# Optimization experiments

Measured on AMD Instinct MI355X. Metric: run time of the kernel, lower is better.

## Reference

```python
import jax, jax.numpy as jnp
import numpy as np

CHANNELS = 128


def setup_inputs() -> dict:
    key = jax.random.key(0)
    ks = jax.random.split(key, 7)
    B, N, C, E = 1, 50000, CHANNELS, 800000
    in_dim = 2 * C + 2  # channels*2 + 2
    tokens = jax.random.normal(ks[0], (B, N, C), dtype=jnp.float32)
    coords = jax.random.normal(ks[1], (B, N, 2), dtype=jnp.float32)
    edge_index = jax.random.randint(ks[2], (2, E), 0, N, dtype=jnp.int64)
    # MLP params: Linear(in_dim, C) -> ReLU -> Linear(C, 1)
    w1 = jax.random.normal(ks[3], (in_dim, C), dtype=jnp.float32) / np.sqrt(in_dim)
    b1 = jnp.zeros((C,), dtype=jnp.float32)
    w2 = jax.random.normal(ks[4], (C, 1), dtype=jnp.float32) / np.sqrt(C)
    b2 = jnp.zeros((1,), dtype=jnp.float32)
    return {"tokens": tokens, "coords": coords, "edge_index": edge_index,
            "w1": w1, "b1": b1, "w2": w2, "b2": b2}


def reference(tokens, coords, edge_index, w1, b1, w2, b2):
    src = edge_index[0]
    dst = edge_index[1]
    x_src = tokens[:, src, :]               # [B, E, C]
    x_dst = tokens[:, dst, :]               # [B, E, C]
    delta = coords[:, dst, :] - coords[:, src, :]  # [B, E, 2]
    feat = jnp.concatenate([x_src, x_dst, delta], axis=-1)  # [B, E, 2C+2]
    h = jax.nn.relu(jnp.einsum('bef,fh->beh', feat, w1) + b1)  # [B, E, C]
    return jnp.einsum('beh,ho->beo', h, w2) + b2               # [B, E, 1]
```

## Files before the change

kernel.cpp:

```cpp
#include <hip/hip_runtime.h>

static constexpr int CH   = 128;
static constexpr int KPAD = 192;

typedef __attribute__((ext_vector_type(8))) short bf16x8;
typedef __attribute__((ext_vector_type(4))) float f32x4;
typedef __attribute__((ext_vector_type(4))) unsigned int u32x4;

__device__ inline unsigned short f2bf(float x) {
    unsigned int u = __float_as_uint(x);
    unsigned int r = (u + 0x7fffu + ((u >> 16) & 1u)) >> 16;
    return (unsigned short)r;
}
__device__ inline unsigned int pack2bf(float a, float b) {
    return (unsigned int)f2bf(a) | ((unsigned int)f2bf(b) << 16);
}

__global__ __launch_bounds__(256) void idx_prep(
    const unsigned int* __restrict__ idxw, uint2* __restrict__ idx2,
    long long E, long long Epad) {
    unsigned nz = 0;
    const int lane = threadIdx.x & 63;
    for (int i = lane; i < 128; i += 64) nz |= idxw[2 * i + 1];
    const int is64 = (__ballot(nz != 0u) == 0ULL) ? 1 : 0;
    const long long stride = (long long)gridDim.x * blockDim.x;
    for (long long i = (long long)blockIdx.x * blockDim.x + threadIdx.x;
         i < Epad; i += stride) {
        uint2 v = make_uint2(0u, 0u);
        if (i < E) {
            const unsigned s = is64 ? idxw[2 * i] : idxw[i];
            const unsigned d = is64 ? idxw[2 * (E + i)] : idxw[E + i];
            v = make_uint2(s << 8, d << 8);
        }
        idx2[i] = v;
    }
}

__global__ __launch_bounds__(256) void w1_prep2(const float* __restrict__ w1,
                                                const float* __restrict__ b1,
                                                unsigned short* __restrict__ Wf) {
    const int gid = blockIdx.x * 256 + threadIdx.x;
    if (gid >= 4 * 5 * 4 * 64) return;
    const int lane = gid & 63;
    const int seg  = gid >> 6;
    const int m    = seg & 3;
    const int ks   = (seg >> 2) % 5;
    const int w    = seg / 20;
    const int c    = w * 64 + m * 16 + (lane & 15);
    const int k0   = ks * 32 + (lane >> 4) * 8;
    const bool isQ = c >= 128;
    const int cc   = c & 127;
    const float sgn = isQ ? 1.f : -1.f;
    unsigned int out[4];
#pragma unroll
    for (int h = 0; h < 4; ++h) {
        float v[2];
#pragma unroll
        for (int j = 0; j < 2; ++j) {
            const int k = k0 + 2 * h + j;
            float x;
            if (k < 128)       x = isQ ? w1[(size_t)(128 + k) * CH + cc]
                                       : w1[(size_t)k * CH + cc];
            else if (k == 128) x = sgn * w1[(size_t)(2 * CH) * CH + cc];
            else if (k == 129) x = sgn * w1[(size_t)(2 * CH + 1) * CH + cc];
            else if (k == 130) x = isQ ? b1[cc] : 0.f;
            else               x = 0.f;
            v[j] = x;
        }
        out[h] = pack2bf(v[0], v[1]);
    }
    *(uint4*)&Wf[(size_t)gid * 8] = make_uint4(out[0], out[1], out[2], out[3]);
}

__global__ __launch_bounds__(256) void node_mfma4(
    const float* __restrict__ tokens, const float* __restrict__ coords,
    const unsigned short* __restrict__ Wf, unsigned short* __restrict__ Pb,
    unsigned short* __restrict__ Qb, int N) {
    __shared__ unsigned short Atile[32 * KPAD];

    const int t    = threadIdx.x;
    const int l    = t & 63;
    const int wid  = t >> 6;
    const int n0   = blockIdx.x * 32;
    const int woff = wid * 64;
    const int bl   = l & 15;
    const int bh   = l >> 4;

#pragma unroll
    for (int it = 0; it < 2; ++it) {
        const int idx  = it * 256 + t;
        const int node = idx >> 4;
        const int cq   = idx & 15;
        float4 v0 = make_float4(0.f, 0.f, 0.f, 0.f);
        float4 v1 = v0;
        if (n0 + node < N) {
            const float* src = &tokens[(size_t)(n0 + node) * CH + cq * 8];
            v0 = *(const float4*)src;
            v1 = *(const float4*)(src + 4);
        }
        uint4 u;
        u.x = pack2bf(v0.x, v0.y);
        u.y = pack2bf(v0.z, v0.w);
        u.z = pack2bf(v1.x, v1.y);
        u.w = pack2bf(v1.z, v1.w);
        const int byte = node * 384 + ((cq * 16) ^ ((node & 7) << 4));
        *(uint4*)((char*)Atile + byte) = u;
    }
    {
        const int node = t >> 3;
        const int ce   = t & 7;
        uint4 u = make_uint4(0u, 0u, 0u, 0u);
        if (ce == 0 && n0 + node < N) {
            const float cx = coords[2 * (n0 + node)];
            const float cy = coords[2 * (n0 + node) + 1];
            u.x = pack2bf(cx, cy);
            u.y = pack2bf(1.f, 0.f);
        }
        const int byte = node * 384 + (((16 + ce) * 16) ^ ((node & 7) << 4));
        *(uint4*)((char*)Atile + byte) = u;
    }
    __syncthreads();

    f32x4 acc[4][2];
#pragma unroll
    for (int m = 0; m < 4; ++m)
#pragma unroll
        for (int n = 0; n < 2; ++n) acc[m][n] = (f32x4){0.f, 0.f, 0.f, 0.f};

#pragma unroll
    for (int ks = 0; ks < 5; ++ks) {
        bf16x8 wfrag[4], tfrag[2];
#pragma unroll
        for (int m = 0; m < 4; ++m)
            wfrag[m] = *(const bf16x8*)&Wf[(size_t)(((wid * 5 + ks) * 4 + m) * 64
                                                    + l) * 8];
#pragma unroll
        for (int n = 0; n < 2; ++n) {
            const int row  = n * 16 + bl;
            const int byte = row * 384 + ((ks * 64 + bh * 16) ^ ((row & 7) << 4));
            tfrag[n] = *(const bf16x8*)((const char*)Atile + byte);
        }
#pragma unroll
        for (int m = 0; m < 4; ++m)
#pragma unroll
            for (int n = 0; n < 2; ++n)
                acc[m][n] = __builtin_amdgcn_mfma_f32_16x16x32_bf16(
                    wfrag[m], tfrag[n], acc[m][n], 0, 0, 0);
    }

#pragma unroll
    for (int m = 0; m < 4; ++m) {
        const int c  = woff + m * 16 + bh * 4;
        const int cc = c & (CH - 1);
        unsigned short* dst = (c < CH) ? Pb : Qb;
#pragma unroll
        for (int n = 0; n < 2; ++n) {
            const int node = n0 + n * 16 + bl;
            if (node < N) {
                uint2 val;
                val.x = pack2bf(acc[m][n][0], acc[m][n][1]);
                val.y = pack2bf(acc[m][n][2], acc[m][n][3]);
                *(uint2*)&dst[(size_t)node * CH + cc] = val;
            }
        }
    }
}

__global__ __launch_bounds__(256) void edge_g16x8(
    const unsigned int* __restrict__ idx2, const char* __restrict__ Pb,
    const char* __restrict__ Qb, const float* __restrict__ w2,
    const float* __restrict__ b2, float* __restrict__ out, long long E) {
    const int t  = threadIdx.x;
    const int gl = t & 15;
    const long long nch = (E + 7) >> 3;
    const long long g0  = (long long)blockIdx.x * 16 + (t >> 4);
    const long long ng  = (long long)gridDim.x * 16;
    const float4 w2a = *(const float4*)&w2[8 * gl];
    const float4 w2b = *(const float4*)&w2[8 * gl + 4];
    const float bias = b2[0];

    for (long long chk = g0; chk < nch; chk += ng) {
        const long long e0 = chk << 3;
        const u32x4* ip = (const u32x4*)&idx2[e0 * 2];
        const u32x4 i0 = __builtin_nontemporal_load(ip);
        const u32x4 i1 = __builtin_nontemporal_load(ip + 1);
        const u32x4 i2 = __builtin_nontemporal_load(ip + 2);
        const u32x4 i3 = __builtin_nontemporal_load(ip + 3);
        const unsigned soff[8] = {i0.x, i0.z, i1.x, i1.z, i2.x, i2.z, i3.x, i3.z};
        const unsigned doff[8] = {i0.y, i0.w, i1.y, i1.w, i2.y, i2.w, i3.y, i3.w};
        uint4 pv[8], qv[8];
#pragma unroll
        for (int j = 0; j < 8; ++j)
            pv[j] = *(const uint4*)(Pb + soff[j] + 16 * gl);
#pragma unroll
        for (int j = 0; j < 8; ++j)
            qv[j] = *(const uint4*)(Qb + doff[j] + 16 * gl);

        float part[8];
#pragma unroll
        for (int j = 0; j < 8; ++j) {
            float acc = 0.f;
            const unsigned pw[4] = {pv[j].x, pv[j].y, pv[j].z, pv[j].w};
            const unsigned qw[4] = {qv[j].x, qv[j].y, qv[j].z, qv[j].w};
            const float wv[8] = {w2a.x, w2a.y, w2a.z, w2a.w,
                                 w2b.x, w2b.y, w2b.z, w2b.w};
#pragma unroll
            for (int wdx = 0; wdx < 4; ++wdx) {
                const float plo = __uint_as_float(pw[wdx] << 16);
                const float phi = __uint_as_float(pw[wdx] & 0xffff0000u);
                const float qlo = __uint_as_float(qw[wdx] << 16);
                const float qhi = __uint_as_float(qw[wdx] & 0xffff0000u);
                const float hlo = fmaxf(plo + qlo, 0.f);
                const float hhi = fmaxf(phi + qhi, 0.f);
                acc = fmaf(hlo, wv[2 * wdx], acc);
                acc = fmaf(hhi, wv[2 * wdx + 1], acc);
            }
            part[j] = acc;
        }

        float t0 = part[0] + __shfl_xor(part[0], 1);
        float t1 = part[1] + __shfl_xor(part[1], 1);
        float t2 = part[2] + __shfl_xor(part[2], 1);
        float t3 = part[3] + __shfl_xor(part[3], 1);
        float t4 = part[4] + __shfl_xor(part[4], 1);
        float t5 = part[5] + __shfl_xor(part[5], 1);
        float t6 = part[6] + __shfl_xor(part[6], 1);
        float t7 = part[7] + __shfl_xor(part[7], 1);
        float a0 = (gl & 1) ? t1 : t0;
        float a1 = (gl & 1) ? t3 : t2;
        float a2 = (gl & 1) ? t5 : t4;
        float a3 = (gl & 1) ? t7 : t6;
        a0 += __shfl_xor(a0, 2);
        a1 += __shfl_xor(a1, 2);
        a2 += __shfl_xor(a2, 2);
        a3 += __shfl_xor(a3, 2);
        float b0  = (gl & 2) ? a1 : a0;
        float b1v = (gl & 2) ? a3 : a2;
        b0  += __shfl_xor(b0, 4);
        b1v += __shfl_xor(b1v, 4);
        float c = (gl & 4) ? b1v : b0;
        c += __shfl_xor(c, 8);

        if (gl < 8 && e0 + gl < E) out[e0 + gl] = c + bias;
    }
}

extern "C" void kernel_launch(void* const* d_in, const int* in_sizes, int n_in,
                              void* d_out, int out_size, void* d_ws,
                              size_t ws_size, hipStream_t stream) {
    const float* tokens = (const float*)d_in[0];
    const float* coords = (const float*)d_in[1];
    const unsigned int* idxw = (const unsigned int*)d_in[2];
    const float* w1 = (const float*)d_in[3];
    const float* b1 = (const float*)d_in[4];
    const float* w2 = (const float*)d_in[5];
    const float* b2 = (const float*)d_in[6];
    float* out = (float*)d_out;

    const int N = in_sizes[0] / CH;
    const long long E = in_sizes[2] / 2;
    const long long Epad = ((E + 7) >> 3) << 3;

    unsigned short* Pb = (unsigned short*)d_ws;
    unsigned short* Qb = Pb + (size_t)N * CH;
    uint2* idx2 = (uint2*)(Qb + (size_t)N * CH);
    unsigned short* Wf = (unsigned short*)(idx2 + Epad);

    idx_prep<<<1024, 256, 0, stream>>>(idxw, idx2, E, Epad);
    w1_prep2<<<20, 256, 0, stream>>>(w1, b1, Wf);

    node_mfma4<<<(N + 31) / 32, 256, 0, stream>>>(tokens, coords, Wf, Pb, Qb, N);

    edge_g16x8<<<2048, 256, 0, stream>>>((const unsigned int*)idx2,
                                         (const char*)Pb, (const char*)Qb,
                                         w2, b2, out, E);
}
```

Baseline: 81.59 us.

## Split node features into channel halves and gather edges in two passes

Node projections P and Q are written as two 64-channel halves each, and the edge kernel runs twice, once per half, accumulating through a partial buffer. The aim is a smaller random-gather working set per pass for better cache hit rates. In exchange, the index array is read twice, an extra launch is added, and a partial-sum buffer is written and reread.

Measured after the change: 77.45 us. 1.05x faster.

```diff
diff --git a/kernel.cpp b/kernel.cpp
--- a/kernel.cpp
+++ b/kernel.cpp
@@ -5,7 +5,7 @@
 
 typedef __attribute__((ext_vector_type(8))) short bf16x8;
 typedef __attribute__((ext_vector_type(4))) float f32x4;
-typedef __attribute__((ext_vector_type(4))) unsigned int u32x4;
+typedef __attribute__((ext_vector_type(2))) unsigned int u32x2;
 
 __device__ inline unsigned short f2bf(float x) {
     unsigned int u = __float_as_uint(x);
@@ -30,7 +30,7 @@
         if (i < E) {
             const unsigned s = is64 ? idxw[2 * i] : idxw[i];
             const unsigned d = is64 ? idxw[2 * (E + i)] : idxw[E + i];
-            v = make_uint2(s << 8, d << 8);
+            v = make_uint2(s << 7, d << 7);
         }
         idx2[i] = v;
     }
@@ -72,17 +72,17 @@
     *(uint4*)&Wf[(size_t)gid * 8] = make_uint4(out[0], out[1], out[2], out[3]);
 }
 
-__global__ __launch_bounds__(256) void node_mfma4(
+__global__ __launch_bounds__(256) void node_mfma5(
     const float* __restrict__ tokens, const float* __restrict__ coords,
-    const unsigned short* __restrict__ Wf, unsigned short* __restrict__ Pb,
-    unsigned short* __restrict__ Qb, int N) {
+    const unsigned short* __restrict__ Wf, unsigned short* __restrict__ Plo,
+    unsigned short* __restrict__ Phi, unsigned short* __restrict__ Qlo,
+    unsigned short* __restrict__ Qhi, int N) {
     __shared__ unsigned short Atile[32 * KPAD];
 
     const int t    = threadIdx.x;
     const int l    = t & 63;
     const int wid  = t >> 6;
     const int n0   = blockIdx.x * 32;
-    const int woff = wid * 64;
     const int bl   = l & 15;
     const int bh   = l >> 4;
 
@@ -148,11 +148,11 @@
                     wfrag[m], tfrag[n], acc[m][n], 0, 0, 0);
     }
 
+    unsigned short* dst = (wid == 0) ? Plo : (wid == 1) ? Phi
+                          : (wid == 2) ? Qlo : Qhi;
 #pragma unroll
     for (int m = 0; m < 4; ++m) {
-        const int c  = woff + m * 16 + bh * 4;
-        const int cc = c & (CH - 1);
-        unsigned short* dst = (c < CH) ? Pb : Qb;
+        const int col = m * 16 + bh * 4;
 #pragma unroll
         for (int n = 0; n < 2; ++n) {
             const int node = n0 + n * 16 + bl;
@@ -160,60 +160,62 @@
                 uint2 val;
                 val.x = pack2bf(acc[m][n][0], acc[m][n][1]);
                 val.y = pack2bf(acc[m][n][2], acc[m][n][3]);
-                *(uint2*)&dst[(size_t)node * CH + cc] = val;
+                *(uint2*)&dst[(size_t)node * 64 + col] = val;
             }
         }
     }
 }
 
-__global__ __launch_bounds__(256) void edge_g16x8(
-    const unsigned int* __restrict__ idx2, const char* __restrict__ Pb,
-    const char* __restrict__ Qb, const float* __restrict__ w2,
-    const float* __restrict__ b2, float* __restrict__ out, long long E) {
+template <int PASS>
+__global__ __launch_bounds__(256) void edge_pass(
+    const unsigned int* __restrict__ idx2w, const unsigned short* __restrict__ Pb,
+    const unsigned short* __restrict__ Qb, const float* __restrict__ w2,
+    const float* __restrict__ b2, float* __restrict__ partial,
+    float* __restrict__ out, long long E) {
     const int t  = threadIdx.x;
-    const int gl = t & 15;
-    const long long nch = (E + 7) >> 3;
-    const long long g0  = (long long)blockIdx.x * 16 + (t >> 4);
-    const long long ng  = (long long)gridDim.x * 16;
-    const float4 w2a = *(const float4*)&w2[8 * gl];
-    const float4 w2b = *(const float4*)&w2[8 * gl + 4];
+    const int gl = t & 7;
+    const long long nq = (E + 3) >> 2;
+    const long long g0 = (long long)blockIdx.x * 32 + (t >> 3);
+    const long long ng = (long long)gridDim.x * 32;
+    const float4 wa = *(const float4*)&w2[PASS * 64 + gl * 8];
+    const float4 wb = *(const float4*)&w2[PASS * 64 + gl * 8 + 4];
     const float bias = b2[0];
-
-    for (long long chk = g0; chk < nch; chk += ng) {
-        const long long e0 = chk << 3;
-        const u32x4* ip = (const u32x4*)&idx2[e0 * 2];
-        const u32x4 i0 = __builtin_nontemporal_load(ip);
-        const u32x4 i1 = __builtin_nontemporal_load(ip + 1);
-        const u32x4 i2 = __builtin_nontemporal_load(ip + 2);
-        const u32x4 i3 = __builtin_nontemporal_load(ip + 3);
-        const unsigned soff[8] = {i0.x, i0.z, i1.x, i1.z, i2.x, i2.z, i3.x, i3.z};
-        const unsigned doff[8] = {i0.y, i0.w, i1.y, i1.w, i2.y, i2.w, i3.y, i3.w};
-        uint4 pv[8], qv[8];
-#pragma unroll
-        for (int j = 0; j < 8; ++j)
-            pv[j] = *(const uint4*)(Pb + soff[j] + 16 * gl);
-#pragma unroll
-        for (int j = 0; j < 8; ++j)
-            qv[j] = *(const uint4*)(Qb + doff[j] + 16 * gl);
-
-        float part[8];
-#pragma unroll
-        for (int j = 0; j < 8; ++j) {
-            float acc = 0.f;
+    const char* P = (const char*)Pb;
+    const char* Q = (const char*)Qb;
+
+    for (long long q = g0; q < nq; q += ng) {
+        const long long e0 = q << 2;
+        const u32x2 iv = __builtin_nontemporal_load(
+            (const u32x2*)&idx2w[(e0 + (gl & 3)) * 2]);
+        unsigned soff[4], doff[4];
+#pragma unroll
+        for (int j = 0; j < 4; ++j) {
+            soff[j] = __shfl(iv.x, j, 8);
+            doff[j] = __shfl(iv.y, j, 8);
+        }
+        uint4 pv[4], qv[4];
+#pragma unroll
+        for (int j = 0; j < 4; ++j)
+            pv[j] = *(const uint4*)(P + soff[j] + 16 * gl);
+#pragma unroll
+        for (int j = 0; j < 4; ++j)
+            qv[j] = *(const uint4*)(Q + doff[j] + 16 * gl);
+
+        float part[4];
+#pragma unroll
+        for (int j = 0; j < 4; ++j) {
+            const float wv[8] = {wa.x, wa.y, wa.z, wa.w, wb.x, wb.y, wb.z, wb.w};
             const unsigned pw[4] = {pv[j].x, pv[j].y, pv[j].z, pv[j].w};
             const unsigned qw[4] = {qv[j].x, qv[j].y, qv[j].z, qv[j].w};
-            const float wv[8] = {w2a.x, w2a.y, w2a.z, w2a.w,
-                                 w2b.x, w2b.y, w2b.z, w2b.w};
-#pragma unroll
-            for (int wdx = 0; wdx < 4; ++wdx) {
-                const float plo = __uint_as_float(pw[wdx] << 16);
-                const float phi = __uint_as_float(pw[wdx] & 0xffff0000u);
-                const float qlo = __uint_as_float(qw[wdx] << 16);
-                const float qhi = __uint_as_float(qw[wdx] & 0xffff0000u);
-                const float hlo = fmaxf(plo + qlo, 0.f);
-                const float hhi = fmaxf(phi + qhi, 0.f);
-                acc = fmaf(hlo, wv[2 * wdx], acc);
-                acc = fmaf(hhi, wv[2 * wdx + 1], acc);
+            float acc = 0.f;
+#pragma unroll
+            for (int i = 0; i < 4; ++i) {
+                const float plo = __uint_as_float(pw[i] << 16);
+                const float phi = __uint_as_float(pw[i] & 0xffff0000u);
+                const float qlo = __uint_as_float(qw[i] << 16);
+                const float qhi = __uint_as_float(qw[i] & 0xffff0000u);
+                acc = fmaf(fmaxf(plo + qlo, 0.f), wv[2 * i], acc);
+                acc = fmaf(fmaxf(phi + qhi, 0.f), wv[2 * i + 1], acc);
             }
             part[j] = acc;
         }
@@ -222,26 +224,21 @@
         float t1 = part[1] + __shfl_xor(part[1], 1);
         float t2 = part[2] + __shfl_xor(part[2], 1);
         float t3 = part[3] + __shfl_xor(part[3], 1);
-        float t4 = part[4] + __shfl_xor(part[4], 1);
-        float t5 = part[5] + __shfl_xor(part[5], 1);
-        float t6 = part[6] + __shfl_xor(part[6], 1);
-        float t7 = part[7] + __shfl_xor(part[7], 1);
         float a0 = (gl & 1) ? t1 : t0;
         float a1 = (gl & 1) ? t3 : t2;
-        float a2 = (gl & 1) ? t5 : t4;
-        float a3 = (gl & 1) ? t7 : t6;
         a0 += __shfl_xor(a0, 2);
         a1 += __shfl_xor(a1, 2);
-        a2 += __shfl_xor(a2, 2);
-        a3 += __shfl_xor(a3, 2);
-        float b0  = (gl & 2) ? a1 : a0;
-        float b1v = (gl & 2) ? a3 : a2;
-        b0  += __shfl_xor(b0, 4);
-        b1v += __shfl_xor(b1v, 4);
-        float c = (gl & 4) ? b1v : b0;
-        c += __shfl_xor(c, 8);
-
-        if (gl < 8 && e0 + gl < E) out[e0 + gl] = c + bias;
+        float c = (gl & 2) ? a1 : a0;
+        c += __shfl_xor(c, 4);
+
+        const long long e = e0 + gl;
+        if (gl < 4 && e < E) {
+            if (PASS == 0) {
+                __builtin_nontemporal_store(c, &partial[e]);
+            } else {
+                out[e] = __builtin_nontemporal_load(&partial[e]) + c + bias;
+            }
+        }
     }
 }
 
@@ -259,19 +256,24 @@
 
     const int N = in_sizes[0] / CH;
     const long long E = in_sizes[2] / 2;
-    const long long Epad = ((E + 7) >> 3) << 3;
-
-    unsigned short* Pb = (unsigned short*)d_ws;
-    unsigned short* Qb = Pb + (size_t)N * CH;
-    uint2* idx2 = (uint2*)(Qb + (size_t)N * CH);
+    const long long Epad = ((E + 3) >> 2) << 2;
+
+    unsigned short* Plo = (unsigned short*)d_ws;
+    unsigned short* Phi = Plo + (size_t)N * 64;
+    unsigned short* Qlo = Phi + (size_t)N * 64;
+    unsigned short* Qhi = Qlo + (size_t)N * 64;
+    uint2* idx2 = (uint2*)(Qhi + (size_t)N * 64);
     unsigned short* Wf = (unsigned short*)(idx2 + Epad);
+    float* partial = (float*)(Wf + 5120 * 8);
 
     idx_prep<<<1024, 256, 0, stream>>>(idxw, idx2, E, Epad);
     w1_prep2<<<20, 256, 0, stream>>>(w1, b1, Wf);
 
-    node_mfma4<<<(N + 31) / 32, 256, 0, stream>>>(tokens, coords, Wf, Pb, Qb, N);
-
-    edge_g16x8<<<2048, 256, 0, stream>>>((const unsigned int*)idx2,
-                                         (const char*)Pb, (const char*)Qb,
-                                         w2, b2, out, E);
-}
+    node_mfma5<<<(N + 31) / 32, 256, 0, stream>>>(tokens, coords, Wf,
+                                                  Plo, Phi, Qlo, Qhi, N);
+
+    edge_pass<0><<<4096, 256, 0, stream>>>((const unsigned int*)idx2, Plo, Qlo,
+                                           w2, b2, partial, out, E);
+    edge_pass<1><<<4096, 256, 0, stream>>>((const unsigned int*)idx2, Phi, Qhi,
+                                           w2, b2, partial, out, E);
+}
```
